# Kernel tuning notes

Measured on AMD Instinct MI355X. Metric: run time of the kernel, lower is better.

Reference implementation:

```python
import jax, jax.numpy as jnp
import numpy as np

B, S, D = 16, 1024, 512
H, DH = 8, 64  # heads, dim_head


def setup_inputs() -> dict:
    key = jax.random.key(0)
    ks = jax.random.split(key, 7)
    x = jax.random.normal(ks[0], (B, S, D), dtype=jnp.float32)
    # variable sequence lengths in [1, S]
    seq_lens = jnp.maximum(jax.random.randint(ks[1], (B,), 0, S + 1), 1).astype(jnp.int32)
    w_std = 0.02
    Wq = jax.random.normal(ks[2], (D, D), dtype=jnp.float32) * w_std
    Wk = jax.random.normal(ks[3], (D, D), dtype=jnp.float32) * w_std
    Wv = jax.random.normal(ks[4], (D, D), dtype=jnp.float32) * w_std
    Wo = jax.random.normal(ks[5], (D, D), dtype=jnp.float32) * w_std
    bo = jnp.zeros((D,), dtype=jnp.float32)
    return {"x": x, "seq_lens": seq_lens, "Wq": Wq, "Wk": Wk, "Wv": Wv, "Wo": Wo, "bo": bo}


def reference(x, seq_lens, Wq, Wk, Wv, Wo, bo):
    # x: [B, S, D] padded ragged batch; seq_lens: [B] valid token counts.
    # Equivalent to the per-batch SDPA loop over jagged sequences: attention
    # is computed only among the valid tokens of each sequence.
    scale = DH ** -0.5
    q = (x @ Wq).reshape(B, S, H, DH)
    k = (x @ Wk).reshape(B, S, H, DH)
    v = (x @ Wv).reshape(B, S, H, DH)
    scores = jnp.einsum('bqhd,bkhd->bhqk', q, k) * scale  # [B,H,S,S]
    valid = jnp.arange(S)[None, :] < seq_lens[:, None]     # [B,S] token mask
    neg_inf = jnp.finfo(scores.dtype).min
    scores = jnp.where(valid[:, None, None, :], scores, neg_inf)
    attn = jax.nn.softmax(scores, axis=-1)
    out = jnp.einsum('bhqk,bkhd->bqhd', attn, v).reshape(B, S, D)
    out = out @ Wo + bo  # to_out Linear (dropout=0 / eval)
    return out * valid[:, :, None]  # zero padded query positions
```

## Files before the change

kernel.cpp:

```cpp
#include <hip/hip_runtime.h>
#include <hip/hip_bf16.h>

typedef __bf16 bf16_t;
typedef __attribute__((ext_vector_type(4))) __bf16 bf16x4;
typedef __attribute__((ext_vector_type(8))) __bf16 bf16x8;
typedef __attribute__((ext_vector_type(4))) float f32x4;

#define MFMA16(a, b, c) __builtin_amdgcn_mfma_f32_16x16x32_bf16((a), (b), (c), 0, 0, 0)

#define BB 16
#define SS 1024
#define DD 512
#define HH 8
#define DH 64
#define NTOK (BB * SS)

typedef const __attribute__((address_space(1))) void gas_void;
typedef __attribute__((address_space(3))) void las_void;

__device__ __forceinline__ void async_cp16(const void* g, void* l) {
    __builtin_amdgcn_global_load_lds((gas_void*)g, (las_void*)l, 16, 0, 0);
}

__device__ __forceinline__ bf16x8 frag_ld(const char* sm, int row, int kk, int g) {
    int r7 = row & 7;
    int base = row * 128 + ((g & 1) << 3);
    int c0 = ((kk << 2) + (g >> 1)) ^ r7;
    int c1 = ((kk << 2) + 2 + (g >> 1)) ^ r7;
    bf16x4 lo = *(const bf16x4*)(sm + base + (c0 << 4));
    bf16x4 hi = *(const bf16x4*)(sm + base + (c1 << 4));
    return __builtin_shufflevector(lo, hi, 0, 1, 2, 3, 4, 5, 6, 7);
}

__global__ __launch_bounds__(256) void cast_x_k(const float* __restrict__ x,
                                                bf16_t* __restrict__ xb, int n4) {
    int i = blockIdx.x * 256 + threadIdx.x;
    if (i < n4) {
        float4 v = ((const float4*)x)[i];
        bf16x4 o;
        o[0] = (bf16_t)v.x; o[1] = (bf16_t)v.y; o[2] = (bf16_t)v.z; o[3] = (bf16_t)v.w;
        *(bf16x4*)(xb + (size_t)i * 4) = o;
    }
}

__global__ __launch_bounds__(256) void transpose_w_k(const float* __restrict__ W0,
                                                     const float* __restrict__ W1,
                                                     const float* __restrict__ W2,
                                                     const float* __restrict__ W3,
                                                     bf16_t* __restrict__ Wt) {
    __shared__ float t[32][33];
    int z = blockIdx.z;
    const float* W = (z == 0) ? W0 : (z == 1) ? W1 : (z == 2) ? W2 : W3;
    bf16_t* out = Wt + (size_t)z * DD * DD;
    int n0 = blockIdx.x * 32, k0 = blockIdx.y * 32;
    int tx = threadIdx.x, ty = threadIdx.y;
#pragma unroll
    for (int i = 0; i < 32; i += 8)
        t[ty + i][tx] = W[(size_t)(k0 + ty + i) * DD + n0 + tx];
    __syncthreads();
#pragma unroll
    for (int i = 0; i < 32; i += 8)
        out[(size_t)(n0 + ty + i) * DD + k0 + tx] = (bf16_t)t[tx][ty + i];
}

template <int MODE>
__global__ __launch_bounds__(256) void gemm_k(const bf16_t* __restrict__ A,
                                              const bf16_t* __restrict__ WtBase,
                                              bf16_t* __restrict__ oQ,
                                              bf16_t* __restrict__ oK,
                                              bf16_t* __restrict__ oVt,
                                              float* __restrict__ oO,
                                              const float* __restrict__ bo,
                                              const int* __restrict__ seq_lens) {
    __shared__ __align__(16) char smem[32768];
    char* smA = smem;
    char* smB = smem + 16384;
    const int tid = threadIdx.x;
    const int l = tid & 63, w = tid >> 6;
    const int lr = l & 15, g = l >> 4;
    const int bm = blockIdx.x, bn = blockIdx.y;
    const int z = (MODE == 0) ? blockIdx.z : 3;
    const bf16_t* Wt = WtBase + (size_t)z * DD * DD;
    const int row0 = bm * 128;
    const int col0 = bn * 128;
    const int wm = (w >> 1) * 64, wn = (w & 1) * 64;

    f32x4 acc[4][4] = {};

    for (int kt = 0; kt < 8; ++kt) {
        const int k0 = kt * 64;
        __syncthreads();
#pragma unroll
        for (int it = 0; it < 4; ++it) {
            int cl = it * 256 + tid;
            int m = cl >> 3, p = cl & 7, c = p ^ (m & 7);
            async_cp16(A + (size_t)(row0 + m) * DD + k0 + c * 8, smA + cl * 16);
        }
#pragma unroll
        for (int it = 0; it < 4; ++it) {
            int cl = it * 256 + tid;
            int m = cl >> 3, p = cl & 7, c = p ^ (m & 7);
            async_cp16(Wt + (size_t)(col0 + m) * DD + k0 + c * 8, smB + cl * 16);
        }
        __syncthreads();
#pragma unroll
        for (int kk = 0; kk < 2; ++kk) {
            bf16x8 af[4], bfr[4];
#pragma unroll
            for (int i = 0; i < 4; ++i) af[i] = frag_ld(smA, wm + i * 16 + lr, kk, g);
#pragma unroll
            for (int j = 0; j < 4; ++j) bfr[j] = frag_ld(smB, wn + j * 16 + lr, kk, g);
#pragma unroll
            for (int i = 0; i < 4; ++i)
#pragma unroll
                for (int j = 0; j < 4; ++j)
                    acc[i][j] = MFMA16(af[i], bfr[j], acc[i][j]);
        }
    }

    if (MODE == 0) {
        if (z < 2) {
            bf16_t* outp = (z == 0) ? oQ : oK;
#pragma unroll
            for (int i = 0; i < 4; ++i) {
                int mrow = row0 + wm + i * 16 + g * 4;
#pragma unroll
                for (int j = 0; j < 4; ++j) {
                    int n = col0 + wn + j * 16 + lr;
                    int h = n >> 6, dh = n & 63;
#pragma unroll
                    for (int r = 0; r < 4; ++r) {
                        int m = mrow + r;
                        int b = m >> 10, s = m & 1023;
                        outp[((size_t)((b * HH + h) * SS + s)) * DH + dh] =
                            (bf16_t)acc[i][j][r];
                    }
                }
            }
        } else {
            __syncthreads();
            bf16_t* tsm = (bf16_t*)smem;
#pragma unroll
            for (int i = 0; i < 4; ++i)
#pragma unroll
                for (int j = 0; j < 4; ++j)
#pragma unroll
                    for (int r = 0; r < 4; ++r)
                        tsm[(wm + i * 16 + g * 4 + r) * 128 + wn + j * 16 + lr] =
                            (bf16_t)acc[i][j][r];
            __syncthreads();
            int nloc = tid >> 1;
            int mbase = (tid & 1) * 64;
            int n = col0 + nloc;
            int h = n >> 6, dh = n & 63;
            int b = row0 >> 10;
            int s0 = (row0 & 1023) + mbase;
            bf16_t* dst = oVt + ((size_t)((b * HH + h) * DH + dh)) * SS + s0;
#pragma unroll
            for (int mm = 0; mm < 64; mm += 8) {
                bf16x8 v;
#pragma unroll
                for (int e = 0; e < 8; ++e) v[e] = tsm[(mbase + mm + e) * 128 + nloc];
                *(bf16x8*)(dst + mm) = v;
            }
        }
    } else {
        int b = row0 >> 10;
        int len = seq_lens[b];
#pragma unroll
        for (int i = 0; i < 4; ++i) {
            int mrow = row0 + wm + i * 16 + g * 4;
#pragma unroll
            for (int j = 0; j < 4; ++j) {
                int n = col0 + wn + j * 16 + lr;
                float bias = bo[n];
#pragma unroll
                for (int r = 0; r < 4; ++r) {
                    int m = mrow + r;
                    int s = m & 1023;
                    oO[(size_t)m * DD + n] = (s < len) ? (acc[i][j][r] + bias) : 0.f;
                }
            }
        }
    }
}

__global__ __launch_bounds__(256) void attn_k(const bf16_t* __restrict__ Q,
                                              const bf16_t* __restrict__ K,
                                              const bf16_t* __restrict__ Vt,
                                              bf16_t* __restrict__ O,
                                              const int* __restrict__ seq_lens) {
    __shared__ __align__(16) char smem[32768];
    const int tid = threadIdx.x, l = tid & 63, w = tid >> 6;
    const int bh = blockIdx.x & 127, qt = blockIdx.x >> 7;
    const int b = bh >> 3, h = bh & 7;
    const int len = seq_lens[b];
    const int q0 = qt * 128;
    if (q0 >= len) return;
    const int lr = l & 15, g = l >> 4;

    const bf16_t* kbase = K + (size_t)bh * SS * DH;
    const bf16_t* vbase = Vt + (size_t)bh * DH * SS;

    bf16x8 bq[2][2];
#pragma unroll
    for (int qs = 0; qs < 2; ++qs) {
        const bf16_t* qp = Q + ((size_t)bh * SS + q0 + w * 32 + qs * 16 + lr) * DH;
#pragma unroll
        for (int kk = 0; kk < 2; ++kk) {
            bf16x4 lo = *(const bf16x4*)(qp + kk * 32 + 4 * g);
            bf16x4 hi = *(const bf16x4*)(qp + kk * 32 + 16 + 4 * g);
            bq[qs][kk] = __builtin_shufflevector(lo, hi, 0, 1, 2, 3, 4, 5, 6, 7);
        }
    }

    f32x4 oacc[2][4] = {};
    float mrun[2] = {-1e30f, -1e30f};
    float lpart[2] = {0.f, 0.f};

    const int nkt = (len + 63) >> 6;

    auto stage = [&](int buf, int key0) {
        char* smK = smem + buf * 16384;
        char* smV = smK + 8192;
#pragma unroll
        for (int it = 0; it < 2; ++it) {
            int cl = it * 256 + tid;
            int m = cl >> 3, p = cl & 7, c = p ^ (m & 7);
            async_cp16(kbase + (size_t)(key0 + m) * DH + c * 8, smK + cl * 16);
        }
#pragma unroll
        for (int it = 0; it < 2; ++it) {
            int cl = it * 256 + tid;
            int m = cl >> 3, p = cl & 7, c = p ^ (m & 7);
            async_cp16(vbase + (size_t)m * SS + key0 + c * 8, smV + cl * 16);
        }
    };

    stage(0, 0);
    __syncthreads();

    for (int kt = 0; kt < nkt; ++kt) {
        const int key0 = kt * 64;
        const char* smK = smem + (kt & 1) * 16384;
        const char* smV = smK + 8192;
        if (kt + 1 < nkt) stage((kt + 1) & 1, key0 + 64);

        f32x4 pacc[2][4] = {};
#pragma unroll
        for (int nt = 0; nt < 4; ++nt) {
            bf16x8 ak0 = frag_ld(smK, nt * 16 + lr, 0, g);
            bf16x8 ak1 = frag_ld(smK, nt * 16 + lr, 1, g);
#pragma unroll
            for (int qs = 0; qs < 2; ++qs) {
                pacc[qs][nt] = MFMA16(ak0, bq[qs][0], pacc[qs][nt]);
                pacc[qs][nt] = MFMA16(ak1, bq[qs][1], pacc[qs][nt]);
            }
        }

#pragma unroll
        for (int qs = 0; qs < 2; ++qs) {
            float mloc = -1e30f;
#pragma unroll
            for (int nt = 0; nt < 4; ++nt)
#pragma unroll
                for (int r = 0; r < 4; ++r) {
                    int kg = key0 + nt * 16 + 4 * g + r;
                    float s = pacc[qs][nt][r] * 0.125f;
                    s = (kg < len) ? s : -1e30f;
                    pacc[qs][nt][r] = s;
                    mloc = fmaxf(mloc, s);
                }
            mloc = fmaxf(mloc, __shfl_xor(mloc, 16, 64));
            mloc = fmaxf(mloc, __shfl_xor(mloc, 32, 64));
            float mn = fmaxf(mrun[qs], mloc);
            float corr = __expf(mrun[qs] - mn);
            mrun[qs] = mn;
            float ls = 0.f;
#pragma unroll
            for (int nt = 0; nt < 4; ++nt)
#pragma unroll
                for (int r = 0; r < 4; ++r) {
                    float p = __expf(pacc[qs][nt][r] - mn);
                    pacc[qs][nt][r] = p;
                    ls += p;
                }
            lpart[qs] = lpart[qs] * corr + ls;
            float cb[4];
#pragma unroll
            for (int r = 0; r < 4; ++r) cb[r] = __shfl(corr, 4 * g + r, 64);
#pragma unroll
            for (int dt = 0; dt < 4; ++dt)
#pragma unroll
                for (int r = 0; r < 4; ++r) oacc[qs][dt][r] *= cb[r];
            bf16x8 pa[2];
#pragma unroll
            for (int kf = 0; kf < 2; ++kf)
#pragma unroll
                for (int j = 0; j < 8; ++j)
                    pa[kf][j] = (bf16_t)pacc[qs][2 * kf + (j >> 2)][j & 3];
#pragma unroll
            for (int kf = 0; kf < 2; ++kf)
#pragma unroll
                for (int dt = 0; dt < 4; ++dt) {
                    bf16x8 bv = frag_ld(smV, dt * 16 + lr, kf, g);
                    oacc[qs][dt] = MFMA16(pa[kf], bv, oacc[qs][dt]);
                }
        }
        __syncthreads();
    }

#pragma unroll
    for (int qs = 0; qs < 2; ++qs) {
        float lt = lpart[qs];
        lt += __shfl_xor(lt, 16, 64);
        lt += __shfl_xor(lt, 32, 64);
#pragma unroll
        for (int r = 0; r < 4; ++r) {
            float inv = 1.f / __shfl(lt, 4 * g + r, 64);
            int q = q0 + w * 32 + qs * 16 + 4 * g + r;
            size_t orow = ((size_t)b * SS + q) * DD;
#pragma unroll
            for (int dt = 0; dt < 4; ++dt)
                O[orow + h * DH + dt * 16 + lr] = (bf16_t)(oacc[qs][dt][r] * inv);
        }
    }
}

extern "C" void kernel_launch(void* const* d_in, const int* in_sizes, int n_in,
                              void* d_out, int out_size, void* d_ws, size_t ws_size,
                              hipStream_t stream) {
    const float* x = (const float*)d_in[0];
    const int* seq_lens = (const int*)d_in[1];
    const float* Wq = (const float*)d_in[2];
    const float* Wk = (const float*)d_in[3];
    const float* Wv = (const float*)d_in[4];
    const float* Wo = (const float*)d_in[5];
    const float* bo = (const float*)d_in[6];
    float* out = (float*)d_out;

    char* ws = (char*)d_ws;
    const size_t SEG = (size_t)NTOK * DD * sizeof(bf16_t);
    bf16_t* xb = (bf16_t*)ws;
    bf16_t* qb = (bf16_t*)(ws + SEG);
    bf16_t* kb = (bf16_t*)(ws + 2 * SEG);
    bf16_t* vtb = (bf16_t*)(ws + 3 * SEG);
    bf16_t* wt = (bf16_t*)(ws + 4 * SEG);
    bf16_t* ab = xb;

    cast_x_k<<<dim3((NTOK * DD / 4) / 256), dim3(256), 0, stream>>>(x, xb, NTOK * DD / 4);
    transpose_w_k<<<dim3(16, 16, 4), dim3(32, 8), 0, stream>>>(Wq, Wk, Wv, Wo, wt);
    gemm_k<0><<<dim3(NTOK / 128, DD / 128, 3), dim3(256), 0, stream>>>(
        xb, wt, qb, kb, vtb, nullptr, nullptr, nullptr);
    attn_k<<<dim3(BB * HH * (SS / 128)), dim3(256), 0, stream>>>(qb, kb, vtb, ab, seq_lens);
    gemm_k<2><<<dim3(NTOK / 128, DD / 128, 1), dim3(256), 0, stream>>>(
        ab, wt, nullptr, nullptr, nullptr, out, bo, seq_lens);
}
```

Measured before the change: 132.1 us.

## Fold softmax scale and log2e into Q projection, skip masking and rescale when unneeded

The Q projection epilogue now multiplies by scale*log2(e), so the attention kernel can use exp2 directly without a per-score multiply. Key masking is skipped for fully valid key tiles, and the running-max correction (exp, shuffles, accumulator rescale) is skipped when no lane's max grows. Block-to-(batch,head,qtile) mapping is also reordered so neighbouring blocks share a batch. This trims VALU work in the softmax inner loop, at the cost of wave-level branches and a slight bf16 rounding change in Q.

```diff
diff --git a/kernel.cpp b/kernel.cpp
--- a/kernel.cpp
+++ b/kernel.cpp
@@ -14,6 +14,7 @@
 #define HH 8
 #define DH 64
 #define NTOK (BB * SS)
+#define QSCALE 0.18033688f
 
 typedef const __attribute__((address_space(1))) void gas_void;
 typedef __attribute__((address_space(3))) void las_void;
@@ -121,6 +122,7 @@
     if (MODE == 0) {
         if (z < 2) {
             bf16_t* outp = (z == 0) ? oQ : oK;
+            const float sc = (z == 0) ? QSCALE : 1.f;
 #pragma unroll
             for (int i = 0; i < 4; ++i) {
                 int mrow = row0 + wm + i * 16 + g * 4;
@@ -133,7 +135,7 @@
                         int m = mrow + r;
                         int b = m >> 10, s = m & 1023;
                         outp[((size_t)((b * HH + h) * SS + s)) * DH + dh] =
-                            (bf16_t)acc[i][j][r];
+                            (bf16_t)(acc[i][j][r] * sc);
                     }
                 }
             }
@@ -192,7 +194,9 @@
                                               const int* __restrict__ seq_lens) {
     __shared__ __align__(16) char smem[32768];
     const int tid = threadIdx.x, l = tid & 63, w = tid >> 6;
-    const int bh = blockIdx.x & 127, qt = blockIdx.x >> 7;
+    const int o = blockIdx.x;
+    const int bh = ((o >> 6) << 3) | (o & 7);
+    const int qt = (o >> 3) & 7;
     const int b = bh >> 3, h = bh & 7;
     const int len = seq_lens[b];
     const int q0 = qt * 128;
@@ -258,41 +262,58 @@
             }
         }
 
+        const bool full = (key0 + 64 <= len);
+
 #pragma unroll
         for (int qs = 0; qs < 2; ++qs) {
             float mloc = -1e30f;
-#pragma unroll
-            for (int nt = 0; nt < 4; ++nt)
-#pragma unroll
-                for (int r = 0; r < 4; ++r) {
-                    int kg = key0 + nt * 16 + 4 * g + r;
-                    float s = pacc[qs][nt][r] * 0.125f;
-                    s = (kg < len) ? s : -1e30f;
-                    pacc[qs][nt][r] = s;
-                    mloc = fmaxf(mloc, s);
-                }
+            if (full) {
+#pragma unroll
+                for (int nt = 0; nt < 4; ++nt)
+#pragma unroll
+                    for (int r = 0; r < 4; ++r) mloc = fmaxf(mloc, pacc[qs][nt][r]);
+            } else {
+#pragma unroll
+                for (int nt = 0; nt < 4; ++nt)
+#pragma unroll
+                    for (int r = 0; r < 4; ++r) {
+                        int kg = key0 + nt * 16 + 4 * g + r;
+                        float s = (kg < len) ? pacc[qs][nt][r] : -1e30f;
+                        pacc[qs][nt][r] = s;
+                        mloc = fmaxf(mloc, s);
+                    }
+            }
             mloc = fmaxf(mloc, __shfl_xor(mloc, 16, 64));
             mloc = fmaxf(mloc, __shfl_xor(mloc, 32, 64));
-            float mn = fmaxf(mrun[qs], mloc);
-            float corr = __expf(mrun[qs] - mn);
-            mrun[qs] = mn;
+
+            float mn;
+            if (__all(mloc <= mrun[qs])) {
+                mn = mrun[qs];
+            } else {
+                mn = fmaxf(mrun[qs], mloc);
+                float corr = __builtin_amdgcn_exp2f(mrun[qs] - mn);
+                mrun[qs] = mn;
+                lpart[qs] *= corr;
+                float cb[4];
+#pragma unroll
+                for (int r = 0; r < 4; ++r) cb[r] = __shfl(corr, 4 * g + r, 64);
+#pragma unroll
+                for (int dt = 0; dt < 4; ++dt)
+#pragma unroll
+                    for (int r = 0; r < 4; ++r) oacc[qs][dt][r] *= cb[r];
+            }
+
             float ls = 0.f;
 #pragma unroll
             for (int nt = 0; nt < 4; ++nt)
 #pragma unroll
                 for (int r = 0; r < 4; ++r) {
-                    float p = __expf(pacc[qs][nt][r] - mn);
+                    float p = __builtin_amdgcn_exp2f(pacc[qs][nt][r] - mn);
                     pacc[qs][nt][r] = p;
                     ls += p;
                 }
-            lpart[qs] = lpart[qs] * corr + ls;
-            float cb[4];
-#pragma unroll
-            for (int r = 0; r < 4; ++r) cb[r] = __shfl(corr, 4 * g + r, 64);
-#pragma unroll
-            for (int dt = 0; dt < 4; ++dt)
-#pragma unroll
-                for (int r = 0; r < 4; ++r) oacc[qs][dt][r] *= cb[r];
+            lpart[qs] += ls;
+
             bf16x8 pa[2];
 #pragma unroll
             for (int kf = 0; kf < 2; ++kf)
```

Result: no change. 129.8 us (-1.8%).
